# Performance work log

Measured on AMD Instinct MI355X. Metric: run time of the kernel, lower is better.

The kernel has to match this reference:

```python
import jax, jax.numpy as jnp
import numpy as np

EMBED_DIM = 128
NUM_HEADS = 8
HEAD_DIM = EMBED_DIM // NUM_HEADS
SCALE = float(np.sqrt(HEAD_DIM))


def setup_inputs() -> dict:
    key = jax.random.key(0)
    ks = jax.random.split(key, 16)
    B, N, M, E = 16, 256, 256, EMBED_DIM
    s = 1.0 / np.sqrt(E)
    inp = {
        "query": jax.random.normal(ks[0], (B, N, E), jnp.float32),
        "key": jax.random.normal(ks[1], (B, M, E), jnp.float32),
        "value": jax.random.normal(ks[2], (B, M, E), jnp.float32),
        "rel_pe": jax.random.normal(ks[3], (B, N, M, E), jnp.float32),
        "attn_mask": jnp.zeros((B, N, M), jnp.float32),
        # linear params stored as [in, out]; y = x @ W + b
        "Wq": jax.random.normal(ks[4], (E, E), jnp.float32) * s,
        "bq": jnp.zeros((E,), jnp.float32),
        "Wk": jax.random.normal(ks[5], (E, E), jnp.float32) * s,
        "bk": jnp.zeros((E,), jnp.float32),
        "Wv": jax.random.normal(ks[6], (E, E), jnp.float32) * s,
        "bv": jnp.zeros((E,), jnp.float32),
        "Wpe": jax.random.normal(ks[7], (E, E), jnp.float32) * s,
        "bpe": jnp.zeros((E,), jnp.float32),
        "Wo": jax.random.normal(ks[8], (E, E), jnp.float32) * s,
        "bo": jnp.zeros((E,), jnp.float32),
    }
    return inp


def reference(query, key, value, rel_pe, attn_mask,
              Wq, bq, Wk, bk, Wv, bv, Wpe, bpe, Wo, bo):
    B, N, E = query.shape
    M = key.shape[1]
    H, D = NUM_HEADS, HEAD_DIM
    q = (query @ Wq + bq).reshape(B, N, H, D)
    k = (key @ Wk + bk).reshape(B, M, H, D)
    v = (value @ Wv + bv).reshape(B, M, H, D)
    pe = (rel_pe @ Wpe + bpe).reshape(B, N, M, H, D)
    score = jnp.einsum('bnhd,bmhd->bhnm', q, k) \
          + jnp.einsum('bnhd,bnmhd->bhnm', q, pe)
    score = score / SCALE + attn_mask[:, None, :, :]
    attn = jax.nn.softmax(score, axis=-1)
    attn = jnp.nan_to_num(attn, nan=0.0)  # dropout is identity in eval mode
    out = jnp.einsum('bhnm,bmhd->bnhd', attn, v) \
        + jnp.einsum('bhnm,bnmhd->bnhd', attn, pe)
    out = out.reshape(B, N, E)
    return out @ Wo + bo
```

## Files before the change

### kernel.cpp

```cpp
#include <hip/hip_runtime.h>
#include <hip/hip_bf16.h>
#include <math.h>

typedef __attribute__((ext_vector_type(8))) short bf16x8;
typedef __attribute__((ext_vector_type(4))) float f32x4;

__device__ __forceinline__ float bf2f_bits(unsigned short u) {
    union { float f; unsigned int i; } x; x.i = ((unsigned int)u) << 16; return x.f;
}

__global__ void qkv_proj_kernel(const float* __restrict__ query,
                                const float* __restrict__ key,
                                const float* __restrict__ value,
                                const float* __restrict__ Wq, const float* __restrict__ bq,
                                const float* __restrict__ Wk, const float* __restrict__ bk,
                                const float* __restrict__ Wv, const float* __restrict__ bv,
                                float* __restrict__ qf, float* __restrict__ kf,
                                float* __restrict__ vf)
{
    const int mat = blockIdx.x >> 8;
    const int rb  = blockIdx.x & 255;
    const float* X; const float* W; const float* bias; float* dst;
    if (mat == 0)      { X = query; W = Wq; bias = bq; dst = qf; }
    else if (mat == 1) { X = key;   W = Wk; bias = bk; dst = kf; }
    else               { X = value; W = Wv; bias = bv; dst = vf; }

    __shared__ float sX[16][128];
    const int tid = threadIdx.x;
    const float* src = X + (size_t)rb * 16 * 128;
    #pragma unroll
    for (int i = 0; i < 8; ++i) {
        int idx = tid + i * 256;
        sX[idx >> 7][idx & 127] = src[idx];
    }
    __syncthreads();

    const int col = tid & 127;
    const int rg  = tid >> 7;
    float acc[8] = {0.f,0.f,0.f,0.f,0.f,0.f,0.f,0.f};
    for (int e = 0; e < 128; ++e) {
        float w = W[e * 128 + col];
        #pragma unroll
        for (int r = 0; r < 8; ++r) acc[r] += sX[rg * 8 + r][e] * w;
    }
    float bb = bias[col];
    #pragma unroll
    for (int r = 0; r < 8; ++r)
        dst[(size_t)(rb * 16 + rg * 8 + r) * 128 + col] = acc[r] + bb;
}

__global__ __launch_bounds__(256) void mha_main_kernel(
    const float* __restrict__ relpe,
    const float* __restrict__ mask,
    const float* __restrict__ qf,
    const float* __restrict__ kf,
    const float* __restrict__ vf,
    const float* __restrict__ Wpe, const float* __restrict__ bpe,
    const float* __restrict__ Wo,  const float* __restrict__ bo,
    float* __restrict__ out)
{
    __shared__ __hip_bfloat16 sW[128][136];
    __shared__ __hip_bfloat16 sA[64][136];
    __shared__ float sP[8][64];
    __shared__ float sQ[128];
    __shared__ float sBpe[128];
    __shared__ float sM[8], sL[8], sR[8];
    __shared__ float sRed[128];
    __shared__ float sOut[128];

    const int tid  = threadIdx.x;
    const int lane = tid & 63;
    const int wv   = tid >> 6;
    const int b    = blockIdx.x >> 8;
    const int n    = blockIdx.x & 255;

    for (int i = 0; i < 64; ++i) {
        int idx = tid + i * 256;
        int k = idx >> 7, o = idx & 127;
        sW[o][k] = __float2bfloat16(Wpe[idx]);
    }
    if (tid < 128) {
        sQ[tid]   = qf[((size_t)(b * 256 + n)) * 128 + tid];
        sBpe[tid] = bpe[tid];
    }
    if (tid < 8) { sM[tid] = -INFINITY; sL[tid] = 0.f; }

    float out_acc = 0.f;
    const int e     = tid & 127;
    const int halfp = tid >> 7;
    const int hh    = e >> 4;
    const int hsc   = tid >> 5;
    const int ml    = tid & 31;
    __syncthreads();

    for (int t = 0; t < 4; ++t) {
        const float4* src4 =
            (const float4*)(relpe + (((size_t)(b * 256 + n)) * 256 + t * 64) * 128);
        #pragma unroll
        for (int i = 0; i < 8; ++i) {
            int idx4 = tid + i * 256;
            float4 v = src4[idx4];
            int lr = idx4 >> 5;
            int c4 = (idx4 & 31) * 4;
            __hip_bfloat162* dp = (__hip_bfloat162*)&sA[lr][c4];
            dp[0] = __float22bfloat162_rn(make_float2(v.x, v.y));
            dp[1] = __float22bfloat162_rn(make_float2(v.z, v.w));
        }
        __syncthreads();

        f32x4 acc[8] = {};
        #pragma unroll
        for (int kt = 0; kt < 4; ++kt) {
            bf16x8 af = *(const bf16x8*)&sA[wv * 16 + (lane & 15)][kt * 32 + (lane >> 4) * 8];
            #pragma unroll
            for (int nt = 0; nt < 8; ++nt) {
                bf16x8 bfr = *(const bf16x8*)&sW[nt * 16 + (lane & 15)][kt * 32 + (lane >> 4) * 8];
                acc[nt] = __builtin_amdgcn_mfma_f32_16x16x32_bf16(af, bfr, acc[nt], 0, 0, 0);
            }
        }
        __syncthreads();

        #pragma unroll
        for (int nt = 0; nt < 8; ++nt) {
            int ee = nt * 16 + (lane & 15);
            float bv_ = sBpe[ee];
            #pragma unroll
            for (int r = 0; r < 4; ++r) {
                int row = wv * 16 + (lane >> 4) * 4 + r;
                sA[row][ee] = __float2bfloat16(acc[nt][r] + bv_);
            }
        }
        __syncthreads();

        float sc[2];
        #pragma unroll
        for (int hf = 0; hf < 2; ++hf) {
            int lr = ml + hf * 32;
            const float4* k4 =
                (const float4*)(kf + ((size_t)(b * 256) + t * 64 + lr) * 128 + hsc * 16);
            float kvv[16];
            ((float4*)kvv)[0] = k4[0];
            ((float4*)kvv)[1] = k4[1];
            ((float4*)kvv)[2] = k4[2];
            ((float4*)kvv)[3] = k4[3];
            const bf16x8* p8 = (const bf16x8*)&sA[lr][hsc * 16];
            bf16x8 pa = p8[0], pb = p8[1];
            const float* qh = &sQ[hsc * 16];
            float s = 0.f;
            #pragma unroll
            for (int d = 0; d < 8; ++d)
                s += qh[d] * (kvv[d] + bf2f_bits((unsigned short)pa[d]));
            #pragma unroll
            for (int d = 0; d < 8; ++d)
                s += qh[8 + d] * (kvv[8 + d] + bf2f_bits((unsigned short)pb[d]));
            sc[hf] = s * 0.25f
                   + mask[(((size_t)(b * 256 + n)) * 256) + t * 64 + lr];
        }

        float tm = fmaxf(sc[0], sc[1]);
        #pragma unroll
        for (int msk = 16; msk >= 1; msk >>= 1)
            tm = fmaxf(tm, __shfl_xor(tm, msk, 32));
        float mold = sM[hsc];
        float mnew = fmaxf(mold, tm);
        float p0 = __expf(sc[0] - mnew);
        float p1 = __expf(sc[1] - mnew);
        float ts = p0 + p1;
        #pragma unroll
        for (int msk = 16; msk >= 1; msk >>= 1)
            ts += __shfl_xor(ts, msk, 32);
        if (ml == 0) {
            float rf = __expf(mold - mnew);
            sR[hsc] = rf;
            sM[hsc] = mnew;
            sL[hsc] = sL[hsc] * rf + ts;
        }
        sP[hsc][ml]      = p0;
        sP[hsc][ml + 32] = p1;
        __syncthreads();

        out_acc *= sR[hh];
        const float* vp = vf + ((size_t)(b * 256) + t * 64 + halfp * 32) * 128 + e;
        #pragma unroll 8
        for (int mm = 0; mm < 32; ++mm) {
            int lr = halfp * 32 + mm;
            out_acc += sP[hh][lr] * (vp[(size_t)mm * 128] + __bfloat162float(sA[lr][e]));
        }
        __syncthreads();
    }

    if (halfp == 1) sRed[e] = out_acc;
    __syncthreads();
    if (halfp == 0) sOut[e] = (out_acc + sRed[e]) / sL[hh];
    __syncthreads();

    float y = 0.f;
    {
        const float* wo = Wo + (size_t)halfp * 64 * 128 + e;
        #pragma unroll 8
        for (int ee = 0; ee < 64; ++ee)
            y += sOut[halfp * 64 + ee] * wo[(size_t)ee * 128];
    }
    if (halfp == 1) sRed[e] = y;
    __syncthreads();
    if (halfp == 0)
        out[((size_t)(b * 256 + n)) * 128 + e] = y + sRed[e] + bo[e];
}

extern "C" void kernel_launch(void* const* d_in, const int* in_sizes, int n_in,
                              void* d_out, int out_size, void* d_ws, size_t ws_size,
                              hipStream_t stream)
{
    const float* query = (const float*)d_in[0];
    const float* key   = (const float*)d_in[1];
    const float* value = (const float*)d_in[2];
    const float* relpe = (const float*)d_in[3];
    const float* mask  = (const float*)d_in[4];
    const float* Wq  = (const float*)d_in[5];
    const float* bq  = (const float*)d_in[6];
    const float* Wk  = (const float*)d_in[7];
    const float* bk  = (const float*)d_in[8];
    const float* Wv  = (const float*)d_in[9];
    const float* bv  = (const float*)d_in[10];
    const float* Wpe = (const float*)d_in[11];
    const float* bpe = (const float*)d_in[12];
    const float* Wo  = (const float*)d_in[13];
    const float* bo  = (const float*)d_in[14];
    float* out = (float*)d_out;

    float* qf = (float*)d_ws;
    float* kf = qf + 16 * 256 * 128;
    float* vf = kf + 16 * 256 * 128;

    qkv_proj_kernel<<<dim3(768), dim3(256), 0, stream>>>(
        query, key, value, Wq, bq, Wk, bk, Wv, bv, qf, kf, vf);
    mha_main_kernel<<<dim3(4096), dim3(256), 0, stream>>>(
        relpe, mask, qf, kf, vf, Wpe, bpe, Wo, bo, out);
}
```

Measured before the change: 260.1 us.

## Fold Wpe projection into query and attention weights instead of projecting rel_pe

```diff
diff --git a/kernel.cpp b/kernel.cpp
--- a/kernel.cpp
+++ b/kernel.cpp
@@ -4,10 +4,6 @@
 
 typedef __attribute__((ext_vector_type(8))) short bf16x8;
 typedef __attribute__((ext_vector_type(4))) float f32x4;
-
-__device__ __forceinline__ float bf2f_bits(unsigned short u) {
-    union { float f; unsigned int i; } x; x.i = ((unsigned int)u) << 16; return x.f;
-}
 
 __global__ void qkv_proj_kernel(const float* __restrict__ query,
                                 const float* __restrict__ key,
@@ -49,7 +45,7 @@
         dst[(size_t)(rb * 16 + rg * 8 + r) * 128 + col] = acc[r] + bb;
 }
 
-__global__ __launch_bounds__(256) void mha_main_kernel(
+__global__ __launch_bounds__(256, 4) void mha_main_kernel(
     const float* __restrict__ relpe,
     const float* __restrict__ mask,
     const float* __restrict__ qf,
@@ -59,12 +55,16 @@
     const float* __restrict__ Wo,  const float* __restrict__ bo,
     float* __restrict__ out)
 {
-    __shared__ __hip_bfloat16 sW[128][136];
     __shared__ __hip_bfloat16 sA[64][136];
-    __shared__ float sP[8][64];
-    __shared__ float sQ[128];
-    __shared__ float sBpe[128];
-    __shared__ float sM[8], sL[8], sR[8];
+    __shared__ __hip_bfloat16 sWt[16][136];
+    __shared__ __hip_bfloat16 sPb[16][72];
+    __shared__ float sSc[64][9];
+    __shared__ float sPf[8][68];
+    __shared__ float sPr[8][132];
+    __shared__ float sQs[128];
+    __shared__ float sCb[8];
+    __shared__ float sM[8], sL[8];
+    __shared__ float sRf[16];
     __shared__ float sRed[128];
     __shared__ float sOut[128];
 
@@ -73,138 +73,201 @@
     const int wv   = tid >> 6;
     const int b    = blockIdx.x >> 8;
     const int n    = blockIdx.x & 255;
-
-    for (int i = 0; i < 64; ++i) {
-        int idx = tid + i * 256;
-        int k = idx >> 7, o = idx & 127;
-        sW[o][k] = __float2bfloat16(Wpe[idx]);
+    const size_t bn = (size_t)(b * 256 + n);
+
+    float4 pf[8];
+    {
+        const float4* s4 = (const float4*)(relpe + (bn * 256) * 128);
+        #pragma unroll
+        for (int i = 0; i < 8; ++i) pf[i] = s4[tid + i * 256];
+    }
+
+    if (tid < 128) sQs[tid] = qf[bn * 128 + tid] * 0.25f;
+    if (tid < 8)  { sM[tid] = -INFINITY; sL[tid] = 0.f; }
+    if (tid < 16) sRf[tid] = 1.f;
+    if (tid < 72) {
+        #pragma unroll
+        for (int r = 8; r < 16; ++r) sPb[r][tid] = __float2bfloat16(0.f);
+    }
+    __syncthreads();
+
+    #pragma unroll
+    for (int o = tid; o < 1024; o += 256) {
+        int h = o >> 7, e = o & 127;
+        const float4* wr = (const float4*)(Wpe + (size_t)e * 128 + h * 16);
+        float4 w0 = wr[0], w1 = wr[1], w2 = wr[2], w3 = wr[3];
+        const float* qh = &sQs[h * 16];
+        float acc = w0.x*qh[0]+w0.y*qh[1]+w0.z*qh[2]+w0.w*qh[3]
+                  + w1.x*qh[4]+w1.y*qh[5]+w1.z*qh[6]+w1.w*qh[7]
+                  + w2.x*qh[8]+w2.y*qh[9]+w2.z*qh[10]+w2.w*qh[11]
+                  + w3.x*qh[12]+w3.y*qh[13]+w3.z*qh[14]+w3.w*qh[15];
+        sWt[h][e] = __float2bfloat16(acc);
     }
     if (tid < 128) {
-        sQ[tid]   = qf[((size_t)(b * 256 + n)) * 128 + tid];
-        sBpe[tid] = bpe[tid];
-    }
-    if (tid < 8) { sM[tid] = -INFINITY; sL[tid] = 0.f; }
+        #pragma unroll
+        for (int r = 8; r < 16; ++r) sWt[r][tid] = __float2bfloat16(0.f);
+    }
+    if (tid < 8) {
+        float acc = 0.f;
+        #pragma unroll
+        for (int d = 0; d < 16; ++d) acc += bpe[tid * 16 + d] * sQs[tid * 16 + d];
+        sCb[tid] = acc;
+    }
+
+    #pragma unroll
+    for (int i = 0; i < 8; ++i) {
+        int idx4 = tid + i * 256;
+        int lr = idx4 >> 5, c4 = (idx4 & 31) * 4;
+        __hip_bfloat162* dp = (__hip_bfloat162*)&sA[lr][c4];
+        dp[0] = __float22bfloat162_rn(make_float2(pf[i].x, pf[i].y));
+        dp[1] = __float22bfloat162_rn(make_float2(pf[i].z, pf[i].w));
+    }
+    __syncthreads();
 
     float out_acc = 0.f;
+    f32x4 pr0 = {}, pr1 = {};
     const int e     = tid & 127;
     const int halfp = tid >> 7;
     const int hh    = e >> 4;
     const int hsc   = tid >> 5;
     const int ml    = tid & 31;
-    __syncthreads();
+    const int arow  = lane & 15;
+    const int koff  = lane >> 4;
 
     for (int t = 0; t < 4; ++t) {
-        const float4* src4 =
-            (const float4*)(relpe + (((size_t)(b * 256 + n)) * 256 + t * 64) * 128);
-        #pragma unroll
-        for (int i = 0; i < 8; ++i) {
-            int idx4 = tid + i * 256;
-            float4 v = src4[idx4];
-            int lr = idx4 >> 5;
-            int c4 = (idx4 & 31) * 4;
-            __hip_bfloat162* dp = (__hip_bfloat162*)&sA[lr][c4];
-            dp[0] = __float22bfloat162_rn(make_float2(v.x, v.y));
-            dp[1] = __float22bfloat162_rn(make_float2(v.z, v.w));
+        if (t < 3) {
+            const float4* s4 = (const float4*)(relpe + (bn * 256 + (t + 1) * 64) * 128);
+            #pragma unroll
+            for (int i = 0; i < 8; ++i) pf[i] = s4[tid + i * 256];
+        }
+
+        f32x4 cs = {};
+        #pragma unroll
+        for (int kt = 0; kt < 4; ++kt) {
+            bf16x8 af  = *(const bf16x8*)&sA[wv * 16 + arow][kt * 32 + koff * 8];
+            bf16x8 bfr = *(const bf16x8*)&sWt[arow][kt * 32 + koff * 8];
+            cs = __builtin_amdgcn_mfma_f32_16x16x32_bf16(af, bfr, cs, 0, 0, 0);
+        }
+        if (arow < 8) {
+            #pragma unroll
+            for (int r = 0; r < 4; ++r) sSc[wv * 16 + koff * 4 + r][arow] = cs[r];
         }
         __syncthreads();
 
-        f32x4 acc[8] = {};
-        #pragma unroll
-        for (int kt = 0; kt < 4; ++kt) {
-            bf16x8 af = *(const bf16x8*)&sA[wv * 16 + (lane & 15)][kt * 32 + (lane >> 4) * 8];
-            #pragma unroll
-            for (int nt = 0; nt < 8; ++nt) {
-                bf16x8 bfr = *(const bf16x8*)&sW[nt * 16 + (lane & 15)][kt * 32 + (lane >> 4) * 8];
-                acc[nt] = __builtin_amdgcn_mfma_f32_16x16x32_bf16(af, bfr, acc[nt], 0, 0, 0);
-            }
+        {
+            float sc[2];
+            #pragma unroll
+            for (int hf = 0; hf < 2; ++hf) {
+                int lr = ml + hf * 32;
+                const float4* k4 =
+                    (const float4*)(kf + ((size_t)(b * 256) + t * 64 + lr) * 128 + hsc * 16);
+                float4 ka = k4[0], kb = k4[1], kc = k4[2], kd = k4[3];
+                const float* qh = &sQs[hsc * 16];
+                float s = sSc[lr][hsc] + sCb[hsc];
+                s += ka.x*qh[0]+ka.y*qh[1]+ka.z*qh[2]+ka.w*qh[3]
+                   + kb.x*qh[4]+kb.y*qh[5]+kb.z*qh[6]+kb.w*qh[7]
+                   + kc.x*qh[8]+kc.y*qh[9]+kc.z*qh[10]+kc.w*qh[11]
+                   + kd.x*qh[12]+kd.y*qh[13]+kd.z*qh[14]+kd.w*qh[15];
+                sc[hf] = s + mask[bn * 256 + t * 64 + lr];
+            }
+            float tm = fmaxf(sc[0], sc[1]);
+            #pragma unroll
+            for (int m2 = 16; m2 >= 1; m2 >>= 1) tm = fmaxf(tm, __shfl_xor(tm, m2, 32));
+            float mold = sM[hsc];
+            float mnew = fmaxf(mold, tm);
+            float p0 = __expf(sc[0] - mnew), p1 = __expf(sc[1] - mnew);
+            float ts = p0 + p1;
+            #pragma unroll
+            for (int m2 = 16; m2 >= 1; m2 >>= 1) ts += __shfl_xor(ts, m2, 32);
+            if (ml == 0) {
+                float rf = __expf(mold - mnew);
+                sRf[hsc] = rf;
+                sM[hsc]  = mnew;
+                sL[hsc]  = sL[hsc] * rf + ts;
+            }
+            sPf[hsc][ml]      = p0;
+            sPf[hsc][ml + 32] = p1;
+            sPb[hsc][ml]      = __float2bfloat16(p0);
+            sPb[hsc][ml + 32] = __float2bfloat16(p1);
         }
         __syncthreads();
 
-        #pragma unroll
-        for (int nt = 0; nt < 8; ++nt) {
-            int ee = nt * 16 + (lane & 15);
-            float bv_ = sBpe[ee];
+        {
             #pragma unroll
             for (int r = 0; r < 4; ++r) {
-                int row = wv * 16 + (lane >> 4) * 4 + r;
-                sA[row][ee] = __float2bfloat16(acc[nt][r] + bv_);
-            }
+                float rf = sRf[koff * 4 + r];
+                pr0[r] *= rf; pr1[r] *= rf;
+            }
+            #pragma unroll
+            for (int kt = 0; kt < 2; ++kt) {
+                bf16x8 ap = *(const bf16x8*)&sPb[arow][kt * 32 + koff * 8];
+                bf16x8 b0, b1;
+                #pragma unroll
+                for (int j = 0; j < 8; ++j) {
+                    int row = kt * 32 + koff * 8 + j;
+                    b0[j] = *(const short*)&sA[row][wv * 32 + arow];
+                    b1[j] = *(const short*)&sA[row][wv * 32 + 16 + arow];
+                }
+                pr0 = __builtin_amdgcn_mfma_f32_16x16x32_bf16(ap, b0, pr0, 0, 0, 0);
+                pr1 = __builtin_amdgcn_mfma_f32_16x16x32_bf16(ap, b1, pr1, 0, 0, 0);
+            }
+            out_acc *= sRf[hh];
+            const float* vp = vf + ((size_t)(b * 256) + t * 64 + halfp * 32) * 128 + e;
+            const float* pp = &sPf[hh][halfp * 32];
+            #pragma unroll 8
+            for (int mm = 0; mm < 32; ++mm)
+                out_acc += pp[mm] * vp[(size_t)mm * 128];
         }
         __syncthreads();
 
-        float sc[2];
-        #pragma unroll
-        for (int hf = 0; hf < 2; ++hf) {
-            int lr = ml + hf * 32;
-            const float4* k4 =
-                (const float4*)(kf + ((size_t)(b * 256) + t * 64 + lr) * 128 + hsc * 16);
-            float kvv[16];
-            ((float4*)kvv)[0] = k4[0];
-            ((float4*)kvv)[1] = k4[1];
-            ((float4*)kvv)[2] = k4[2];
-            ((float4*)kvv)[3] = k4[3];
-            const bf16x8* p8 = (const bf16x8*)&sA[lr][hsc * 16];
-            bf16x8 pa = p8[0], pb = p8[1];
-            const float* qh = &sQ[hsc * 16];
-            float s = 0.f;
-            #pragma unroll
-            for (int d = 0; d < 8; ++d)
-                s += qh[d] * (kvv[d] + bf2f_bits((unsigned short)pa[d]));
-            #pragma unroll
-            for (int d = 0; d < 8; ++d)
-                s += qh[8 + d] * (kvv[8 + d] + bf2f_bits((unsigned short)pb[d]));
-            sc[hf] = s * 0.25f
-                   + mask[(((size_t)(b * 256 + n)) * 256) + t * 64 + lr];
-        }
-
-        float tm = fmaxf(sc[0], sc[1]);
-        #pragma unroll
-        for (int msk = 16; msk >= 1; msk >>= 1)
-            tm = fmaxf(tm, __shfl_xor(tm, msk, 32));
-        float mold = sM[hsc];
-        float mnew = fmaxf(mold, tm);
-        float p0 = __expf(sc[0] - mnew);
-        float p1 = __expf(sc[1] - mnew);
-        float ts = p0 + p1;
-        #pragma unroll
-        for (int msk = 16; msk >= 1; msk >>= 1)
-            ts += __shfl_xor(ts, msk, 32);
-        if (ml == 0) {
-            float rf = __expf(mold - mnew);
-            sR[hsc] = rf;
-            sM[hsc] = mnew;
-            sL[hsc] = sL[hsc] * rf + ts;
-        }
-        sP[hsc][ml]      = p0;
-        sP[hsc][ml + 32] = p1;
-        __syncthreads();
-
-        out_acc *= sR[hh];
-        const float* vp = vf + ((size_t)(b * 256) + t * 64 + halfp * 32) * 128 + e;
+        if (t < 3) {
+            #pragma unroll
+            for (int i = 0; i < 8; ++i) {
+                int idx4 = tid + i * 256;
+                int lr = idx4 >> 5, c4 = (idx4 & 31) * 4;
+                __hip_bfloat162* dp = (__hip_bfloat162*)&sA[lr][c4];
+                dp[0] = __float22bfloat162_rn(make_float2(pf[i].x, pf[i].y));
+                dp[1] = __float22bfloat162_rn(make_float2(pf[i].z, pf[i].w));
+            }
+            __syncthreads();
+        }
+    }
+
+    if (halfp) sRed[e] = out_acc;
+    __syncthreads();
+    float outv = out_acc + (halfp ? 0.f : sRed[e]);
+
+    #pragma unroll
+    for (int r = 0; r < 4; ++r) {
+        int row = koff * 4 + r;
+        if (row < 8) {
+            sPr[row][wv * 32 + arow]      = pr0[r];
+            sPr[row][wv * 32 + 16 + arow] = pr1[r];
+        }
+    }
+    __syncthreads();
+
+    float ype = 0.f;
+    {
+        const float* wp  = Wpe + (size_t)(halfp * 64) * 128 + e;
+        const float* prh = &sPr[hh][halfp * 64];
         #pragma unroll 8
-        for (int mm = 0; mm < 32; ++mm) {
-            int lr = halfp * 32 + mm;
-            out_acc += sP[hh][lr] * (vp[(size_t)mm * 128] + __bfloat162float(sA[lr][e]));
-        }
-        __syncthreads();
-    }
-
-    if (halfp == 1) sRed[e] = out_acc;
-    __syncthreads();
-    if (halfp == 0) sOut[e] = (out_acc + sRed[e]) / sL[hh];
+        for (int ee = 0; ee < 64; ++ee) ype += prh[ee] * wp[(size_t)ee * 128];
+    }
+    if (halfp) sRed[e] = ype;
+    __syncthreads();
+    if (!halfp) sOut[e] = (outv + ype + sRed[e]) / sL[hh] + bpe[e];
     __syncthreads();
 
     float y = 0.f;
     {
-        const float* wo = Wo + (size_t)halfp * 64 * 128 + e;
+        const float* wo = Wo + (size_t)(halfp * 64) * 128 + e;
         #pragma unroll 8
-        for (int ee = 0; ee < 64; ++ee)
-            y += sOut[halfp * 64 + ee] * wo[(size_t)ee * 128];
-    }
-    if (halfp == 1) sRed[e] = y;
-    __syncthreads();
-    if (halfp == 0)
-        out[((size_t)(b * 256 + n)) * 128 + e] = y + sRed[e] + bo[e];
+        for (int ee = 0; ee < 64; ++ee) y += sOut[halfp * 64 + ee] * wo[(size_t)ee * 128];
+    }
+    if (halfp) sRed[e] = y;
+    __syncthreads();
+    if (!halfp) out[bn * 128 + e] = y + sRed[e] + bo[e];
 }
 
 extern "C" void kernel_launch(void* const* d_in, const int* in_sizes, int n_in,
```

New measurement: 214.3 us. -17.6%, faster.
